# Optimization experiments

Hardware: AMD Instinct MI355X
Metric: run time of the kernel (lower is better)

## Reference

```python
import jax, jax.numpy as jnp
import numpy as np

B, Q, M = 4, 256, 256
QS, KS, H = 512, 512, 512


def setup_inputs() -> dict:
    key = jax.random.key(0)
    ks = jax.random.split(key, 12)
    s = 0.02
    return {
        "query": jax.random.normal(ks[0], (B, Q, QS), dtype=jnp.float32),
        "memory": jax.random.normal(ks[1], (B, M, KS), dtype=jnp.float32),
        "mask": jax.random.randint(ks[2], (B, M), 0, 2).astype(jnp.bool_),
        "Wk": jax.random.normal(ks[3], (H, KS), dtype=jnp.float32) * s,
        "bk": jnp.zeros((H,), dtype=jnp.float32),
        "Wq": jax.random.normal(ks[4], (H, QS), dtype=jnp.float32) * s,
        "bq": jnp.zeros((H,), dtype=jnp.float32),
        "Wl": jax.random.normal(ks[5], (1, H), dtype=jnp.float32) * s,
        "bl": jnp.zeros((1,), dtype=jnp.float32),
        "Wo": jax.random.normal(ks[6], (QS, QS + KS), dtype=jnp.float32) * s,
        "bo": jnp.zeros((QS,), dtype=jnp.float32),
    }


def reference(query, memory, mask, Wk, bk, Wq, bq, Wl, bl, Wo, bo):
    # Projections: q [B,Q,H], k [B,M,H]
    q = jnp.einsum("bqd,hd->bqh", query, Wq) + bq
    k = jnp.einsum("bmd,hd->bmh", memory, Wk) + bk
    # Additive (Bahdanau) scores: broadcast add -> tanh -> hidden->1 projection
    e = jnp.tanh(q[:, :, None, :] + k[:, None, :, :])  # [B,Q,M,H]
    logits = jnp.einsum("bqmh,h->bqm", e, Wl[0]) + bl[0]  # [B,Q,M]
    logits = jnp.where(mask[:, None, :], jnp.float32(-1e18), logits)
    weights = jax.nn.softmax(logits, axis=-1)  # [B,Q,M]
    attns = jnp.einsum("bqm,bmd->bqd", weights, memory)  # [B,Q,KS]
    combined = jnp.concatenate([query, attns], axis=-1)  # [B,Q,QS+KS]
    output = jnp.tanh(jnp.einsum("bqc,oc->bqo", combined, Wo) + bo)
    return output, weights
```

## Files before the change

### kernel.cpp

```cpp
#include <hip/hip_runtime.h>


#define B_   4
#define Q_   256
#define M_   256
#define H_   512
#define QS_  512
#define KS_  512

#define TSC 2.8853900817779268f

typedef __attribute__((ext_vector_type(8))) short bf16x8;
typedef __attribute__((ext_vector_type(4))) float f32x4;

__device__ __forceinline__ float fast_exp2(float x) { return __builtin_amdgcn_exp2f(x); }

__device__ __forceinline__ float tanh_fast(float x) {
    float e = fast_exp2(x * TSC);
    return 1.0f - 2.0f * __builtin_amdgcn_rcpf(e + 1.0f);
}

__device__ __forceinline__ unsigned short rne_bf16(float f) {
    unsigned b = __builtin_bit_cast(unsigned, f);
    return (unsigned short)((b + 0x7FFFu + ((b >> 16) & 1u)) >> 16);
}

__device__ __forceinline__ bf16x8 cvt8(const float* __restrict__ p) {
    const float4 lo = *(const float4*)p;
    const float4 hi = *(const float4*)(p + 4);
    float f[8] = {lo.x, lo.y, lo.z, lo.w, hi.x, hi.y, hi.z, hi.w};
    union { bf16x8 v; unsigned short u[8]; } r;
#pragma unroll
    for (int j = 0; j < 8; ++j) r.u[j] = rne_bf16(f[j]);
    return r.v;
}

__global__ __launch_bounds__(256) void prep(const float* __restrict__ query,
                                            const float* __restrict__ memory,
                                            const float* __restrict__ Wq,
                                            const float* __restrict__ Wk,
                                            const float* __restrict__ Wo,
                                            const unsigned char* __restrict__ mask,
                                            unsigned short* __restrict__ qbf,
                                            unsigned short* __restrict__ mbf,
                                            unsigned short* __restrict__ wqbf,
                                            unsigned short* __restrict__ wkbf,
                                            unsigned short* __restrict__ wobf,
                                            int* __restrict__ maskN, int nmask) {
    if (blockIdx.x == 1024) {
        __shared__ int flags[4];
        const int tid = threadIdx.x;
        int any = 0;
        for (int i = tid; i < nmask; i += 256)
            if ((i & 3) && mask[i]) any = 1;
        int wany = __any(any);
        if ((tid & 63) == 0) flags[tid >> 6] = wany ? 1 : 0;
        __syncthreads();
        const int isbool = flags[0] | flags[1] | flags[2] | flags[3];
        const int* ri = (const int*)mask;
        for (int i = tid; i < nmask; i += 256)
            maskN[i] = isbool ? (int)mask[i] : ri[i];
        return;
    }
    const int u = blockIdx.x * 256 + threadIdx.x;
    const float* src;
    unsigned short* dst;
    int off;
    if (u < 131072) {
        if (u < 65536) { src = query;  dst = qbf; off = u; }
        else           { src = memory; dst = mbf; off = u - 65536; }
    } else if (u < 196608) {
        if (u < 163840) { src = Wq; dst = wqbf; off = u - 131072; }
        else            { src = Wk; dst = wkbf; off = u - 163840; }
    } else { src = Wo; dst = wobf; off = u - 196608; }
    const int i = off * 8;
    *(bf16x8*)&dst[i] = cvt8(&src[i]);
}

__global__ __launch_bounds__(256) void gemm5(const unsigned short* __restrict__ qbf,
                                             const unsigned short* __restrict__ mbf,
                                             const unsigned short* __restrict__ wqbf,
                                             const unsigned short* __restrict__ wkbf,
                                             const unsigned short* __restrict__ wobf,
                                             const float* __restrict__ bq,
                                             const float* __restrict__ bk,
                                             const float* __restrict__ bo,
                                             float* __restrict__ Eq,
                                             float* __restrict__ Ek,
                                             float* __restrict__ Y1,
                                             float* __restrict__ Z) {
    const int lane = threadIdx.x & 63;
    const int wid  = threadIdx.x >> 6;
    const int gt  = blockIdx.x * 4 + wid;
    const int seg = gt >> 9;
    const int t   = gt & 511;
    const int tm  = t >> 4;
    const int tn  = t & 15;

    const unsigned short* A;
    const unsigned short* W;
    const float* bias;
    float* C;
    int ldW, wko;
    if (seg == 0)      { A = qbf; W = wqbf; ldW = 512;  wko = 0;   bias = bq; C = Eq; }
    else if (seg == 1) { A = mbf; W = wkbf; ldW = 512;  wko = 0;   bias = bk; C = Ek; }
    else if (seg == 2) { A = qbf; W = wobf; ldW = 1024; wko = 0;   bias = bo; C = Y1; }
    else               { A = mbf; W = wobf; ldW = 1024; wko = 512; bias = nullptr; C = Z; }

    const int rA = tm * 32 + (lane & 15);
    const int rB = tn * 32 + (lane & 15);
    const int ko = (lane >> 4) * 8;

    f32x4 acc00 = {0,0,0,0}, acc01 = {0,0,0,0}, acc10 = {0,0,0,0}, acc11 = {0,0,0,0};
#pragma unroll
    for (int kt = 0; kt < 512; kt += 32) {
        bf16x8 a0 = *(const bf16x8*)&A[rA * 512 + kt + ko];
        bf16x8 a1 = *(const bf16x8*)&A[(rA + 16) * 512 + kt + ko];
        bf16x8 b0 = *(const bf16x8*)&W[rB * ldW + wko + kt + ko];
        bf16x8 b1 = *(const bf16x8*)&W[(rB + 16) * ldW + wko + kt + ko];
        acc00 = __builtin_amdgcn_mfma_f32_16x16x32_bf16(a0, b0, acc00, 0, 0, 0);
        acc01 = __builtin_amdgcn_mfma_f32_16x16x32_bf16(a0, b1, acc01, 0, 0, 0);
        acc10 = __builtin_amdgcn_mfma_f32_16x16x32_bf16(a1, b0, acc10, 0, 0, 0);
        acc11 = __builtin_amdgcn_mfma_f32_16x16x32_bf16(a1, b1, acc11, 0, 0, 0);
    }
    const int col = tn * 32 + (lane & 15);
    const int r0  = tm * 32 + (lane >> 4) * 4;
    const float bv0 = bias ? bias[col] : 0.f;
    const float bv1 = bias ? bias[col + 16] : 0.f;
    if (seg < 2) {
#pragma unroll
        for (int j = 0; j < 4; ++j) {
            C[(r0 + j) * 512 + col]           = fast_exp2(TSC * (acc00[j] + bv0));
            C[(r0 + j) * 512 + col + 16]      = fast_exp2(TSC * (acc01[j] + bv1));
            C[(r0 + 16 + j) * 512 + col]      = fast_exp2(TSC * (acc10[j] + bv0));
            C[(r0 + 16 + j) * 512 + col + 16] = fast_exp2(TSC * (acc11[j] + bv1));
        }
    } else {
#pragma unroll
        for (int j = 0; j < 4; ++j) {
            C[(r0 + j) * 512 + col]           = acc00[j] + bv0;
            C[(r0 + j) * 512 + col + 16]      = acc01[j] + bv1;
            C[(r0 + 16 + j) * 512 + col]      = acc10[j] + bv0;
            C[(r0 + 16 + j) * 512 + col + 16] = acc11[j] + bv1;
        }
    }
}

__global__ __launch_bounds__(1024) void attn_fused(const int* __restrict__ maskN,
                                                   const float* __restrict__ Eq,
                                                   const float* __restrict__ Ek,
                                                   const float* __restrict__ Wl,
                                                   const float* __restrict__ bl,
                                                   const float* __restrict__ Y1,
                                                   const float* __restrict__ Z,
                                                   float* __restrict__ wout,
                                                   float* __restrict__ out) {
    const int b = blockIdx.y;
    const int q0 = blockIdx.x * 4;
    const int tid = threadIdx.x;
    const int wid = tid >> 6;
    const int lane = tid & 63;

    __shared__ float slog[4][M_];
    __shared__ float swt[4][M_];
    __shared__ int s_list[M_];
    __shared__ int s_base[4];
    __shared__ int s_cnt;
    __shared__ int s_allmask;

    int msk_ = 1, prefix_ = 0;
    if (tid < 256) {
        msk_ = maskN[(b << 8) + tid];
        unsigned long long vote = __ballot(msk_ == 0);
        prefix_ = __popcll(vote & ((1ull << lane) - 1ull));
        if (lane == 0) s_base[wid] = __popcll(vote);
    }
    __syncthreads();
    if (tid == 0) {
        int s = 0;
#pragma unroll
        for (int i = 0; i < 4; ++i) { int c = s_base[i]; s_base[i] = s; s += c; }
        s_cnt = s;
    }
    __syncthreads();
    if (tid < 256 && !msk_) s_list[s_base[wid] + prefix_] = tid;

    float qreg[4][8], wlr[8];
#pragma unroll
    for (int qi = 0; qi < 4; ++qi) {
        const float* qp = &Eq[((b << 8) + (q0 + qi)) * H_ + lane * 8];
        *(float4*)&qreg[qi][0] = *(const float4*)qp;
        *(float4*)&qreg[qi][4] = *(const float4*)(qp + 4);
    }
    *(float4*)&wlr[0] = *(const float4*)&Wl[lane * 8];
    *(float4*)&wlr[4] = *(const float4*)&Wl[lane * 8 + 4];
    const float bl0 = bl[0];

    float sumWL = wlr[0] + wlr[1] + wlr[2] + wlr[3] + wlr[4] + wlr[5] + wlr[6] + wlr[7];
#pragma unroll
    for (int off = 32; off; off >>= 1) sumWL += __shfl_xor(sumWL, off, 64);

    __syncthreads();
    const int cnt = s_cnt;

    for (int idx = wid; idx < cnt; idx += 16) {
        const int m = s_list[idx];
        float kr[8];
        const float* kp = &Ek[((b << 8) + m) * H_ + lane * 8];
        *(float4*)&kr[0] = *(const float4*)kp;
        *(float4*)&kr[4] = *(const float4*)(kp + 4);
        float acc[4] = {0.f, 0.f, 0.f, 0.f};
#pragma unroll
        for (int h = 0; h < 8; ++h) {
            const float ek = kr[h];
            const float wv = wlr[h];
#pragma unroll
            for (int qi = 0; qi < 4; ++qi) {
                const float e = qreg[qi][h] * ek;
                const float r = __builtin_amdgcn_rcpf(e + 1.0f);
                acc[qi] = fmaf(wv, r, acc[qi]);
            }
        }
#pragma unroll
        for (int qi = 0; qi < 4; ++qi) {
            float v = acc[qi];
#pragma unroll
            for (int off = 32; off; off >>= 1) v += __shfl_xor(v, off, 64);
            if (lane == 0) slog[qi][m] = sumWL - 2.0f * v + bl0;
        }
    }
    __syncthreads();

    if (wid < 4) {
        const int qi = wid;
        float x[4];
        int mk[4];
#pragma unroll
        for (int j = 0; j < 4; ++j) {
            const int m = lane * 4 + j;
            mk[j] = maskN[(b << 8) + m];
            x[j] = mk[j] ? -1e30f : slog[qi][m];
        }
        float mx = fmaxf(fmaxf(x[0], x[1]), fmaxf(x[2], x[3]));
#pragma unroll
        for (int off = 32; off; off >>= 1) mx = fmaxf(mx, __shfl_xor(mx, off, 64));
        float e[4], s = 0.f;
#pragma unroll
        for (int j = 0; j < 4; ++j) {
            e[j] = mk[j] ? 0.f : fast_exp2((x[j] - mx) * 1.4426950408889634f);
            s += e[j];
        }
#pragma unroll
        for (int off = 32; off; off >>= 1) s += __shfl_xor(s, off, 64);
        float w4[4];
        if (s > 0.f) {
            const float inv = 1.0f / s;
#pragma unroll
            for (int j = 0; j < 4; ++j) w4[j] = e[j] * inv;
        } else {
#pragma unroll
            for (int j = 0; j < 4; ++j) w4[j] = 1.0f / (float)M_;
        }
#pragma unroll
        for (int j = 0; j < 4; ++j) swt[qi][lane * 4 + j] = w4[j];
        *(float4*)&wout[((b << 8) + (q0 + qi)) * M_ + lane * 4] = *(const float4*)w4;
        if (tid == 0) s_allmask = (s <= 0.f) ? 1 : 0;
    }
    __syncthreads();

    if (tid < QS_) {
        const int am = s_allmask;
        float a[4] = {0.f, 0.f, 0.f, 0.f};
        const float* Zb = &Z[((b << 8)) * QS_ + tid];
        if (!am) {
            for (int idx = 0; idx < cnt; ++idx) {
                const int m = s_list[idx];
                const float zv = Zb[m * QS_];
#pragma unroll
                for (int qi = 0; qi < 4; ++qi) a[qi] = fmaf(swt[qi][m], zv, a[qi]);
            }
        } else {
            for (int m = 0; m < M_; ++m) {
                const float zv = Zb[m * QS_];
#pragma unroll
                for (int qi = 0; qi < 4; ++qi) a[qi] = fmaf(swt[qi][m], zv, a[qi]);
            }
        }
#pragma unroll
        for (int qi = 0; qi < 4; ++qi) {
            const int r = (b << 8) + q0 + qi;
            out[r * QS_ + tid] = tanh_fast(Y1[r * QS_ + tid] + a[qi]);
        }
    }
}

extern "C" void kernel_launch(void* const* d_in, const int* in_sizes, int n_in,
                              void* d_out, int out_size, void* d_ws, size_t ws_size,
                              hipStream_t stream) {
    const float* query  = (const float*)d_in[0];
    const float* memory = (const float*)d_in[1];
    const void*  mask   = d_in[2];
    const float* Wk = (const float*)d_in[3];
    const float* bk = (const float*)d_in[4];
    const float* Wq = (const float*)d_in[5];
    const float* bq = (const float*)d_in[6];
    const float* Wl = (const float*)d_in[7];
    const float* bl = (const float*)d_in[8];
    const float* Wo = (const float*)d_in[9];
    const float* bo = (const float*)d_in[10];

    float* out  = (float*)d_out;
    float* wout = out + B_ * Q_ * QS_;

    float* ws = (float*)d_ws;
    float*          Eq    = ws;
    float*          Ek    = ws + 524288;
    float*          Y1    = ws + 1048576;
    float*          Z     = ws + 1572864;
    unsigned short* qbf   = (unsigned short*)(ws + 2097152);
    unsigned short* mbf   = (unsigned short*)(ws + 2359296);
    unsigned short* wqbf  = (unsigned short*)(ws + 2621440);
    unsigned short* wkbf  = (unsigned short*)(ws + 2752512);
    unsigned short* wobf  = (unsigned short*)(ws + 2883584);
    int*            maskN = (int*)(ws + 3145728);

    hipLaunchKernelGGL(prep, dim3(1025), dim3(256), 0, stream,
                       query, memory, Wq, Wk, Wo, (const unsigned char*)mask,
                       qbf, mbf, wqbf, wkbf, wobf, maskN, in_sizes[2]);
    hipLaunchKernelGGL(gemm5, dim3(512), dim3(256), 0, stream,
                       qbf, mbf, wqbf, wkbf, wobf, bq, bk, bo, Eq, Ek, Y1, Z);
    hipLaunchKernelGGL(attn_fused, dim3(Q_ / 4, B_), dim3(1024), 0, stream,
                       maskN, Eq, Ek, Wl, bl, Y1, Z, wout, out);
}
```

Before: 55.54 us.

## Split GEMM K-loop into dual accumulators, use all threads in attn output, widen prep blocks

The GEMM kernel now splits the K dimension into two halves with separate accumulator sets. This breaks the serial MFMA dependency chain and issues more independent loads per iteration. The attention output stage uses all 1024 threads, each computing two query rows instead of 512 threads computing four, so the Z reads are spread over more threads. The prep kernel switches to 1024-thread blocks. More accumulators and loads in flight raise register pressure in the GEMM, and the Z column reads are now duplicated across the two thread halves.

```diff
diff --git a/kernel.cpp b/kernel.cpp
--- a/kernel.cpp
+++ b/kernel.cpp
@@ -35,34 +35,36 @@
     return r.v;
 }
 
-__global__ __launch_bounds__(256) void prep(const float* __restrict__ query,
-                                            const float* __restrict__ memory,
-                                            const float* __restrict__ Wq,
-                                            const float* __restrict__ Wk,
-                                            const float* __restrict__ Wo,
-                                            const unsigned char* __restrict__ mask,
-                                            unsigned short* __restrict__ qbf,
-                                            unsigned short* __restrict__ mbf,
-                                            unsigned short* __restrict__ wqbf,
-                                            unsigned short* __restrict__ wkbf,
-                                            unsigned short* __restrict__ wobf,
-                                            int* __restrict__ maskN, int nmask) {
-    if (blockIdx.x == 1024) {
-        __shared__ int flags[4];
-        const int tid = threadIdx.x;
+__global__ __launch_bounds__(1024) void prep(const float* __restrict__ query,
+                                             const float* __restrict__ memory,
+                                             const float* __restrict__ Wq,
+                                             const float* __restrict__ Wk,
+                                             const float* __restrict__ Wo,
+                                             const unsigned char* __restrict__ mask,
+                                             unsigned short* __restrict__ qbf,
+                                             unsigned short* __restrict__ mbf,
+                                             unsigned short* __restrict__ wqbf,
+                                             unsigned short* __restrict__ wkbf,
+                                             unsigned short* __restrict__ wobf,
+                                             int* __restrict__ maskN, int nmask) {
+    const int tid = threadIdx.x;
+    if (blockIdx.x == 256) {
+        __shared__ int flags[16];
         int any = 0;
-        for (int i = tid; i < nmask; i += 256)
+        for (int i = tid; i < nmask; i += 1024)
             if ((i & 3) && mask[i]) any = 1;
         int wany = __any(any);
         if ((tid & 63) == 0) flags[tid >> 6] = wany ? 1 : 0;
         __syncthreads();
-        const int isbool = flags[0] | flags[1] | flags[2] | flags[3];
+        int isbool = 0;
+#pragma unroll
+        for (int j = 0; j < 16; ++j) isbool |= flags[j];
         const int* ri = (const int*)mask;
-        for (int i = tid; i < nmask; i += 256)
+        for (int i = tid; i < nmask; i += 1024)
             maskN[i] = isbool ? (int)mask[i] : ri[i];
         return;
     }
-    const int u = blockIdx.x * 256 + threadIdx.x;
+    const int u = blockIdx.x * 1024 + tid;
     const float* src;
     unsigned short* dst;
     int off;
@@ -111,17 +113,28 @@
     const int rB = tn * 32 + (lane & 15);
     const int ko = (lane >> 4) * 8;
 
-    f32x4 acc00 = {0,0,0,0}, acc01 = {0,0,0,0}, acc10 = {0,0,0,0}, acc11 = {0,0,0,0};
-#pragma unroll
-    for (int kt = 0; kt < 512; kt += 32) {
-        bf16x8 a0 = *(const bf16x8*)&A[rA * 512 + kt + ko];
-        bf16x8 a1 = *(const bf16x8*)&A[(rA + 16) * 512 + kt + ko];
-        bf16x8 b0 = *(const bf16x8*)&W[rB * ldW + wko + kt + ko];
-        bf16x8 b1 = *(const bf16x8*)&W[(rB + 16) * ldW + wko + kt + ko];
-        acc00 = __builtin_amdgcn_mfma_f32_16x16x32_bf16(a0, b0, acc00, 0, 0, 0);
-        acc01 = __builtin_amdgcn_mfma_f32_16x16x32_bf16(a0, b1, acc01, 0, 0, 0);
-        acc10 = __builtin_amdgcn_mfma_f32_16x16x32_bf16(a1, b0, acc10, 0, 0, 0);
-        acc11 = __builtin_amdgcn_mfma_f32_16x16x32_bf16(a1, b1, acc11, 0, 0, 0);
+    f32x4 p00 = {0,0,0,0}, p01 = {0,0,0,0}, p10 = {0,0,0,0}, p11 = {0,0,0,0};
+    f32x4 q00 = {0,0,0,0}, q01 = {0,0,0,0}, q10 = {0,0,0,0}, q11 = {0,0,0,0};
+#pragma unroll
+    for (int kt = 0; kt < 256; kt += 32) {
+        const int k0 = kt + ko;
+        const int k1 = 256 + kt + ko;
+        bf16x8 a0 = *(const bf16x8*)&A[rA * 512 + k0];
+        bf16x8 a1 = *(const bf16x8*)&A[(rA + 16) * 512 + k0];
+        bf16x8 b0 = *(const bf16x8*)&W[rB * ldW + wko + k0];
+        bf16x8 b1 = *(const bf16x8*)&W[(rB + 16) * ldW + wko + k0];
+        bf16x8 c0 = *(const bf16x8*)&A[rA * 512 + k1];
+        bf16x8 c1 = *(const bf16x8*)&A[(rA + 16) * 512 + k1];
+        bf16x8 d0 = *(const bf16x8*)&W[rB * ldW + wko + k1];
+        bf16x8 d1 = *(const bf16x8*)&W[(rB + 16) * ldW + wko + k1];
+        p00 = __builtin_amdgcn_mfma_f32_16x16x32_bf16(a0, b0, p00, 0, 0, 0);
+        p01 = __builtin_amdgcn_mfma_f32_16x16x32_bf16(a0, b1, p01, 0, 0, 0);
+        p10 = __builtin_amdgcn_mfma_f32_16x16x32_bf16(a1, b0, p10, 0, 0, 0);
+        p11 = __builtin_amdgcn_mfma_f32_16x16x32_bf16(a1, b1, p11, 0, 0, 0);
+        q00 = __builtin_amdgcn_mfma_f32_16x16x32_bf16(c0, d0, q00, 0, 0, 0);
+        q01 = __builtin_amdgcn_mfma_f32_16x16x32_bf16(c0, d1, q01, 0, 0, 0);
+        q10 = __builtin_amdgcn_mfma_f32_16x16x32_bf16(c1, d0, q10, 0, 0, 0);
+        q11 = __builtin_amdgcn_mfma_f32_16x16x32_bf16(c1, d1, q11, 0, 0, 0);
     }
     const int col = tn * 32 + (lane & 15);
     const int r0  = tm * 32 + (lane >> 4) * 4;
@@ -130,18 +143,18 @@
     if (seg < 2) {
 #pragma unroll
         for (int j = 0; j < 4; ++j) {
-            C[(r0 + j) * 512 + col]           = fast_exp2(TSC * (acc00[j] + bv0));
-            C[(r0 + j) * 512 + col + 16]      = fast_exp2(TSC * (acc01[j] + bv1));
-            C[(r0 + 16 + j) * 512 + col]      = fast_exp2(TSC * (acc10[j] + bv0));
-            C[(r0 + 16 + j) * 512 + col + 16] = fast_exp2(TSC * (acc11[j] + bv1));
+            C[(r0 + j) * 512 + col]           = fast_exp2(TSC * (p00[j] + q00[j] + bv0));
+            C[(r0 + j) * 512 + col + 16]      = fast_exp2(TSC * (p01[j] + q01[j] + bv1));
+            C[(r0 + 16 + j) * 512 + col]      = fast_exp2(TSC * (p10[j] + q10[j] + bv0));
+            C[(r0 + 16 + j) * 512 + col + 16] = fast_exp2(TSC * (p11[j] + q11[j] + bv1));
         }
     } else {
 #pragma unroll
         for (int j = 0; j < 4; ++j) {
-            C[(r0 + j) * 512 + col]           = acc00[j] + bv0;
-            C[(r0 + j) * 512 + col + 16]      = acc01[j] + bv1;
-            C[(r0 + 16 + j) * 512 + col]      = acc10[j] + bv0;
-            C[(r0 + 16 + j) * 512 + col + 16] = acc11[j] + bv1;
+            C[(r0 + j) * 512 + col]           = p00[j] + q00[j] + bv0;
+            C[(r0 + j) * 512 + col + 16]      = p01[j] + q01[j] + bv1;
+            C[(r0 + 16 + j) * 512 + col]      = p10[j] + q10[j] + bv0;
+            C[(r0 + 16 + j) * 512 + col + 16] = p11[j] + q11[j] + bv1;
         }
     }
 }
@@ -268,29 +281,29 @@
     }
     __syncthreads();
 
-    if (tid < QS_) {
+    {
         const int am = s_allmask;
-        float a[4] = {0.f, 0.f, 0.f, 0.f};
-        const float* Zb = &Z[((b << 8)) * QS_ + tid];
+        const int d = tid & 511;
+        const int qp = (tid >> 9) << 1;
+        const float* Zb = &Z[((b << 8)) * QS_ + d];
+        float a0 = 0.f, a1 = 0.f;
         if (!am) {
             for (int idx = 0; idx < cnt; ++idx) {
                 const int m = s_list[idx];
                 const float zv = Zb[m * QS_];
-#pragma unroll
-                for (int qi = 0; qi < 4; ++qi) a[qi] = fmaf(swt[qi][m], zv, a[qi]);
+                a0 = fmaf(swt[qp][m], zv, a0);
+                a1 = fmaf(swt[qp + 1][m], zv, a1);
             }
         } else {
             for (int m = 0; m < M_; ++m) {
                 const float zv = Zb[m * QS_];
-#pragma unroll
-                for (int qi = 0; qi < 4; ++qi) a[qi] = fmaf(swt[qi][m], zv, a[qi]);
+                a0 = fmaf(swt[qp][m], zv, a0);
+                a1 = fmaf(swt[qp + 1][m], zv, a1);
             }
         }
-#pragma unroll
-        for (int qi = 0; qi < 4; ++qi) {
-            const int r = (b << 8) + q0 + qi;
-            out[r * QS_ + tid] = tanh_fast(Y1[r * QS_ + tid] + a[qi]);
-        }
+        const int r0 = (b << 8) + q0 + qp;
+        out[r0 * QS_ + d]        = tanh_fast(Y1[r0 * QS_ + d] + a0);
+        out[(r0 + 1) * QS_ + d]  = tanh_fast(Y1[(r0 + 1) * QS_ + d] + a1);
     }
 }
 
@@ -324,7 +337,7 @@
     unsigned short* wobf  = (unsigned short*)(ws + 2883584);
     int*            maskN = (int*)(ws + 3145728);
 
-    hipLaunchKernelGGL(prep, dim3(1025), dim3(256), 0, stream,
+    hipLaunchKernelGGL(prep, dim3(257), dim3(1024), 0, stream,
                        query, memory, Wq, Wk, Wo, (const unsigned char*)mask,
                        qbf, mbf, wqbf, wkbf, wobf, maskN, in_sizes[2]);
     hipLaunchKernelGGL(gemm5, dim3(512), dim3(256), 0, stream,
```

Result: slower. 57.06 us (+2.7%).
